# Kernel optimization log

Measured on AMD Instinct MI355X. Metric: run time of the kernel, lower is better.

Reference implementation:

```python
import jax, jax.numpy as jnp
import numpy as np

EPS = 1e-6


def _expand_mask(mask, D, H, W):
    # mask: (B,1,f,f,f) bool -> (B,1,D,H,W) via repeat_interleave on each spatial axis
    m = jnp.repeat(mask, D // mask.shape[2], axis=2)
    m = jnp.repeat(m, H // mask.shape[3], axis=3)
    m = jnp.repeat(m, W // mask.shape[4], axis=4)
    return m


def setup_inputs() -> dict:
    key = jax.random.key(0)
    ks = jax.random.split(key, 10)
    B, C, D, H, W = 2, 192, 32, 32, 32
    K, HID = 7, 4 * C
    x = jax.random.normal(ks[0], (B, C, D, H, W), dtype=jnp.float32)
    mask = jax.random.randint(ks[1], (B, 1, 8, 8, 8), 0, 2) > 0
    dw_w = jax.random.normal(ks[2], (C, 1, K, K, K), dtype=jnp.float32) * (1.0 / np.sqrt(K**3))
    dw_b = jnp.zeros((C,), dtype=jnp.float32)
    ln_w = jnp.ones((C,), dtype=jnp.float32)
    ln_b = jnp.zeros((C,), dtype=jnp.float32)
    w1 = jax.random.normal(ks[3], (C, HID), dtype=jnp.float32) * (1.0 / np.sqrt(C))
    b1 = jnp.zeros((HID,), dtype=jnp.float32)
    w2 = jax.random.normal(ks[4], (HID, C), dtype=jnp.float32) * (1.0 / np.sqrt(HID))
    b2 = jnp.zeros((C,), dtype=jnp.float32)
    gamma = jnp.full((C,), 1e-6, dtype=jnp.float32)
    return {"x": x, "mask": mask, "dw_w": dw_w, "dw_b": dw_b, "ln_w": ln_w,
            "ln_b": ln_b, "w1": w1, "b1": b1, "w2": w2, "b2": b2, "gamma": gamma}


def reference(x, mask, dw_w, dw_b, ln_w, ln_b, w1, b1, w2, b2, gamma):
    B, C, D, H, W = x.shape
    m = _expand_mask(mask, D, H, W)              # (B,1,D,H,W) bool
    mf = m.astype(x.dtype)

    # depthwise 3D conv, SAME padding (padding = kernel//2), groups = C
    y = jax.lax.conv_general_dilated(
        x, dw_w, window_strides=(1, 1, 1), padding='SAME',
        dimension_numbers=('NCDHW', 'OIDHW', 'NCDHW'),
        feature_group_count=C)
    y = y + dw_b[None, :, None, None, None]

    # channels_last: (B,D,H,W,C)
    y = jnp.transpose(y, (0, 2, 3, 4, 1))

    # sparse LayerNorm over channel dim: normalize all tokens, keep only active
    # (equivalent to gather->LN->scatter-into-zeros in the original)
    mu = jnp.mean(y, axis=-1, keepdims=True)
    var = jnp.mean(jnp.square(y - mu), axis=-1, keepdims=True)
    ln = (y - mu) * jax.lax.rsqrt(var + EPS) * ln_w + ln_b
    ln = ln * jnp.transpose(mf, (0, 2, 3, 4, 1))  # zero inactive tokens

    # pointwise MLP
    h = jax.nn.gelu(jnp.einsum('bdhwc,ce->bdhwe', ln, w1) + b1, approximate=False)
    o = jnp.einsum('bdhwe,ec->bdhwc', h, w2) + b2
    o = gamma * o

    # back to channels_first and final sparse mask
    o = jnp.transpose(o, (0, 4, 1, 2, 3)) * mf
    return o
```

## Files before the change

### kernel.cpp

```cpp
#include <hip/hip_runtime.h>
#include <hip/hip_bf16.h>

typedef __attribute__((ext_vector_type(2))) float f2v;
typedef __attribute__((ext_vector_type(4))) float f4v;
typedef __attribute__((ext_vector_type(8))) short bf8v;
typedef __attribute__((ext_vector_type(8))) _Float16 h8v;

#define NPOS 32768
#define CCH  192
#define HID  768

#define WS_Y    ((size_t)0)
#define WS_B1F  ((size_t)25165824)
#define WS_B2F  ((size_t)25460736)
#define WS_WPF  ((size_t)25755648)
#define WS_B3F  ((size_t)26056704)
#define WS_TOTAL_MFMA ((size_t)35690496)
#define WS_TOTAL_DOT2 ((size_t)26056704)

__device__ inline unsigned short f2bf(float f){
  unsigned int u = __float_as_uint(f);
  u += 0x7FFFu + ((u >> 16) & 1u);
  return (unsigned short)(u >> 16);
}
__device__ inline float bf2f(unsigned short s){
  return __uint_as_float(((unsigned int)s) << 16);
}
__device__ inline float gelu_f(float x){
  float u = 0.7978845608028654f * x * fmaf(0.044715f, x*x, 1.0f);
  float e = __expf(2.0f*u);
  float th = __fdividef(e - 1.0f, e + 1.0f);
  return 0.5f*x*(1.0f + th);
}

#define DOT2(A, X, W) \
  asm("v_dot2_f32_f16 %0, %1, %2, %0" : "+v"(A) : "v"(X), "s"(W))

__global__ __launch_bounds__(256) void compact_kernel(
    const int* __restrict__ mask, int* __restrict__ list)
{
  __shared__ unsigned short cnt[256];
  __shared__ int pref[257];
  int t = threadIdx.x;
  int m[4], c0 = 0;
  #pragma unroll
  for (int i = 0; i < 4; ++i) { m[i] = mask[t*4 + i]; c0 += (m[i] != 0); }
  cnt[t] = (unsigned short)c0;
  __syncthreads();
  if (t == 0) {
    int s = 0;
    for (int i = 0; i < 256; ++i) { pref[i] = s; s += cnt[i]; }
    pref[256] = s;
  }
  __syncthreads();
  int na = pref[256];
  int pa = pref[t];
  int pi = na + (t*4 - pref[t]);
  #pragma unroll
  for (int i = 0; i < 4; ++i) {
    if (m[i]) list[pa++] = t*4 + i;
    else      list[pi++] = t*4 + i;
  }
  if (t == 0) list[1024] = na;
}

#define ZSTR 712
__global__ __launch_bounds__(256) void conv_mfma_kernel(
    const float* __restrict__ x, const float* __restrict__ dw_b,
    const unsigned short* __restrict__ b3f, unsigned short* __restrict__ yc)
{
  __shared__ unsigned short tile[22*ZSTR];

  int bid = blockIdx.x;
  int c = bid % 192;
  int r = bid / 192;
  int xq = r & 1, yq = (r >> 1) & 1, zh = (r >> 2) & 1, b = r >> 3;
  int tx0 = xq*16, ty0 = yq*16, zb = zh*16;

  int tid = threadIdx.x;
  const float* xsrc = x + ((size_t)(b*CCH + c))*NPOS;

  #pragma unroll
  for (int it = 0; it < 8; ++it) {
    int idx = tid + 256*it;
    if (idx < 1936) {
      int ci = idx & 3;
      int row = idx >> 2;
      int lz = row / 22, ly = row - lz*22;
      int gz = zb - 3 + lz, gy = ty0 - 3 + ly;
      f4v v0 = {0.f,0.f,0.f,0.f}, v1 = {0.f,0.f,0.f,0.f};
      if (((unsigned)gz < 32u) & ((unsigned)gy < 32u) & (ci < 3)) {
        int gx0 = tx0 - 4 + 8*ci;
        const float* src = xsrc + (size_t)gz*1024 + gy*32;
        if ((unsigned)gx0 <= 28u)     v0 = *(const f4v*)(src + gx0);
        if ((unsigned)(gx0+4) <= 28u) v1 = *(const f4v*)(src + gx0 + 4);
      }
      h8v pk;
      pk[0] = (_Float16)v0[0]; pk[1] = (_Float16)v0[1];
      pk[2] = (_Float16)v0[2]; pk[3] = (_Float16)v0[3];
      pk[4] = (_Float16)v1[0]; pk[5] = (_Float16)v1[1];
      pk[6] = (_Float16)v1[2]; pk[7] = (_Float16)v1[3];
      *(h8v*)(tile + lz*ZSTR + ly*32 + ci*8) = pk;
    }
  }
  __syncthreads();

  int wv = tid >> 6, lane = tid & 63;
  int q = lane >> 4, zm = lane & 15;

  const unsigned short* abase = tile + (size_t)zm*ZSTR + q*8;
  const unsigned short* bbase = b3f + ((size_t)c*49)*512 + (size_t)lane*8;

  f4v acc[4];
  #pragma unroll
  for (int t = 0; t < 4; ++t) acc[t] = (f4v){0.f,0.f,0.f,0.f};

  #pragma unroll 1
  for (int kz = 0; kz < 7; ++kz) {
    h8v Bt[7];
    #pragma unroll
    for (int ky = 0; ky < 7; ++ky)
      Bt[ky] = *(const h8v*)(bbase + (size_t)(kz*7 + ky)*512);
    h8v Af[10];
    #pragma unroll
    for (int rr = 0; rr < 10; ++rr)
      Af[rr] = *(const h8v*)(abase + kz*ZSTR + (4*wv + rr)*32);
    #pragma unroll
    for (int ky = 0; ky < 7; ++ky) {
      acc[0] = __builtin_amdgcn_mfma_f32_16x16x32_f16(Af[ky+0], Bt[ky], acc[0], 0, 0, 0);
      acc[1] = __builtin_amdgcn_mfma_f32_16x16x32_f16(Af[ky+1], Bt[ky], acc[1], 0, 0, 0);
      acc[2] = __builtin_amdgcn_mfma_f32_16x16x32_f16(Af[ky+2], Bt[ky], acc[2], 0, 0, 0);
      acc[3] = __builtin_amdgcn_mfma_f32_16x16x32_f16(Af[ky+3], Bt[ky], acc[3], 0, 0, 0);
    }
  }

  float bias = dw_b[c];
  int cz = zh*4 + q;
  int cx = (tx0 >> 2) + (zm >> 2);
  int xr = zm & 3;
  int cy = (ty0 >> 2) + wv;
  int cell = cz*64 + cy*8 + cx;
  unsigned short* yb0 = yc + (((size_t)(b*512 + cell))*192 + c)*64 + xr;
  #pragma unroll
  for (int t = 0; t < 4; ++t) {
    unsigned short* yb = yb0 + t*4;
    yb[0]  = f2bf(acc[t][0] + bias);
    yb[16] = f2bf(acc[t][1] + bias);
    yb[32] = f2bf(acc[t][2] + bias);
    yb[48] = f2bf(acc[t][3] + bias);
  }
}

__global__ __launch_bounds__(256, 6) void conv_dw_f16_kernel(
    const float* __restrict__ x, const float* __restrict__ dw_b,
    const unsigned int* __restrict__ wpf, unsigned short* __restrict__ yc)
{
  __shared__ unsigned short ring[22*528];

  int bid = blockIdx.x;
  int c = bid % 192;
  int r = bid / 192;
  int xq = r & 1, yq = (r >> 1) & 1, zh = (r >> 2) & 1, b = r >> 3;
  int tx0 = xq*16, ty0 = yq*16, zb = zh*16;

  int tid = threadIdx.x;
  const float* xsrc = x + ((size_t)(b*CCH + c))*NPOS;

  for (int idx = tid; idx < 2904; idx += 256) {
    int sl = idx / 132;
    int rem = idx - sl*132;
    int rr = rem / 6, ci = rem - rr*6;
    int zi = zb - 3 + sl, gy = ty0 - 3 + rr, gx = tx0 - 4 + 4*ci;
    f4v v = {0.f, 0.f, 0.f, 0.f};
    if ((unsigned)zi < 32u && (unsigned)gy < 32u && (unsigned)gx <= 28u)
      v = *(const f4v*)(xsrc + (size_t)zi*1024 + gy*32 + gx);
    union { _Float16 h[4]; uint2 u2; } pk;
    pk.h[0] = (_Float16)v[0]; pk.h[1] = (_Float16)v[1];
    pk.h[2] = (_Float16)v[2]; pk.h[3] = (_Float16)v[3];
    *(uint2*)(ring + sl*528 + rr*24 + ci*4) = pk.u2;
  }
  __syncthreads();

  int p = tid & 15, zl = tid >> 4;
  int px = p & 3, py = p >> 2;
  int y0 = py*4, px4 = px*4;
  const unsigned short* base = ring + zl*528 + y0*24 + px4;
  const unsigned int* wb = wpf + (size_t)c*392;

  float acc[4][4];
  #pragma unroll
  for (int i = 0; i < 4; ++i)
    #pragma unroll
    for (int j = 0; j < 4; ++j) acc[i][j] = 0.f;

  #pragma unroll 1
  for (int s = 0; s < 7; ++s) {
    const unsigned short* sb = base + s*528;
    const unsigned int* wrow = wb + s*56;
    #pragma unroll
    for (int rr = 0; rr < 10; ++rr) {
      const unsigned short* rb = sb + rr*24;
      uint2 q0 = *(const uint2*)(rb);
      uint2 q1 = *(const uint2*)(rb + 4);
      uint2 q2 = *(const uint2*)(rb + 8);
      unsigned int D[6] = {q0.x, q0.y, q1.x, q1.y, q2.x, q2.y};
      #pragma unroll
      for (int dy = 0; dy < 4; ++dy) {
        int ky = rr - dy;
        if (ky < 0 || ky > 6) continue;
        const unsigned int* wk = wrow + ky*8;
        #pragma unroll
        for (int t = 0; t < 4; ++t) {
          DOT2(acc[dy][0], D[t],   wk[t]);
          DOT2(acc[dy][1], D[t+1], wk[4+t]);
          DOT2(acc[dy][2], D[t+1], wk[t]);
          DOT2(acc[dy][3], D[t+2], wk[4+t]);
        }
      }
    }
  }

  float bias = dw_b[c];
  int z = zb + zl;
  int cz = z >> 2, cx = (tx0 >> 2) + px, cy = (ty0 >> 2) + py;
  int cell = cz*64 + cy*8 + cx;
  unsigned short* ybase = yc + (((size_t)(b*512 + cell))*192 + c)*64;
  int tokz = (z & 3)*16;
  #pragma unroll
  for (int dy = 0; dy < 4; ++dy) {
    ushort4 o;
    o.x = f2bf(acc[dy][0] + bias);
    o.y = f2bf(acc[dy][1] + bias);
    o.z = f2bf(acc[dy][2] + bias);
    o.w = f2bf(acc[dy][3] + bias);
    *(ushort4*)(ybase + tokz + dy*4) = o;
  }
}

__global__ __launch_bounds__(256) void conv_dw_f32_kernel(
    const float* __restrict__ x, const float* __restrict__ dw_w,
    const float* __restrict__ dw_b, unsigned short* __restrict__ yc)
{
  __shared__ float ring[22*528];

  int bid = blockIdx.x;
  int c = bid % 192;
  int r = bid / 192;
  int xq = r & 1, yq = (r >> 1) & 1, zh = (r >> 2) & 1, b = r >> 3;
  int tx0 = xq*16, ty0 = yq*16, zb = zh*16;

  int tid = threadIdx.x;
  const float* xsrc = x + ((size_t)(b*CCH + c))*NPOS;

  for (int idx = tid; idx < 2904; idx += 256) {
    int sl = idx / 132;
    int rem = idx - sl*132;
    int rr = rem / 6, ci = rem - rr*6;
    int zi = zb - 3 + sl, gy = ty0 - 3 + rr, gx = tx0 - 4 + 4*ci;
    f4v v = {0.f, 0.f, 0.f, 0.f};
    if ((unsigned)zi < 32u && (unsigned)gy < 32u && (unsigned)gx <= 28u)
      v = *(const f4v*)(xsrc + (size_t)zi*1024 + gy*32 + gx);
    *(f4v*)(ring + sl*528 + rr*24 + ci*4) = v;
  }
  __syncthreads();

  int p = tid & 15, zl = tid >> 4;
  int px = p & 3, py = p >> 2;
  int y0 = py*4, px4 = px*4;
  const float* base = ring + zl*528 + y0*24 + px4;
  const float* wbase = dw_w + (size_t)c*343;

  f2v acc[8];
  #pragma unroll
  for (int i = 0; i < 8; ++i) acc[i] = (f2v){0.f, 0.f};

  #pragma unroll 1
  for (int s = 0; s < 7; ++s) {
    const float* sb = base + s*528;
    f4v n0 = *(const f4v*)(sb);
    f4v n1 = *(const f4v*)(sb + 4);
    f4v n2 = *(const f4v*)(sb + 8);
    #pragma unroll
    for (int rr = 0; rr < 10; ++rr) {
      f4v r0 = n0, r1 = n1, r2 = n2;
      if (rr < 9) {
        n0 = *(const f4v*)(sb + (rr+1)*24);
        n1 = *(const f4v*)(sb + (rr+1)*24 + 4);
        n2 = *(const f4v*)(sb + (rr+1)*24 + 8);
      }
      f2v pr[10];
      pr[1] = (f2v){r0[1], r0[2]};
      pr[2] = (f2v){r0[2], r0[3]};
      pr[3] = (f2v){r0[3], r1[0]};
      pr[4] = (f2v){r1[0], r1[1]};
      pr[5] = (f2v){r1[1], r1[2]};
      pr[6] = (f2v){r1[2], r1[3]};
      pr[7] = (f2v){r1[3], r2[0]};
      pr[8] = (f2v){r2[0], r2[1]};
      pr[9] = (f2v){r2[1], r2[2]};
      #pragma unroll
      for (int dy = 0; dy < 4; ++dy) {
        int ky = rr - dy;
        if (ky < 0 || ky > 6) continue;
        #pragma unroll
        for (int kx = 0; kx < 7; ++kx) {
          float w = wbase[s*49 + ky*7 + kx];
          f2v wv = (f2v){w, w};
          acc[dy*2+0] = __builtin_elementwise_fma(wv, pr[kx+1], acc[dy*2+0]);
          acc[dy*2+1] = __builtin_elementwise_fma(wv, pr[kx+3], acc[dy*2+1]);
        }
      }
    }
  }

  float bias = dw_b[c];
  int z = zb + zl;
  int cz = z >> 2, cx = (tx0 >> 2) + px, cy = (ty0 >> 2) + py;
  int cell = cz*64 + cy*8 + cx;
  unsigned short* ybase = yc + (((size_t)(b*512 + cell))*192 + c)*64;
  int tokz = (z & 3)*16;
  #pragma unroll
  for (int dy = 0; dy < 4; ++dy) {
    ushort4 o;
    o.x = f2bf(acc[dy*2+0][0] + bias);
    o.y = f2bf(acc[dy*2+0][1] + bias);
    o.z = f2bf(acc[dy*2+1][0] + bias);
    o.w = f2bf(acc[dy*2+1][1] + bias);
    *(ushort4*)(ybase + tokz + dy*4) = o;
  }
}

__global__ __launch_bounds__(256) void prep_w_kernel(
    const float* __restrict__ w1, const float* __restrict__ w2,
    const float* __restrict__ dw_w,
    unsigned short* __restrict__ b1f, unsigned short* __restrict__ b2f,
    unsigned int* __restrict__ wpf, unsigned short* __restrict__ b3f)
{
  int gid = blockIdx.x*256 + threadIdx.x;
  if (gid < 18432) {
    int fi = gid;
    int lane = fi & 63, fr = fi >> 6;
    int nt = fr / 6, ks = fr - nt*6;
    int n  = nt*16 + (lane & 15);
    int kb = ks*32 + (lane >> 4)*8;
    #pragma unroll
    for (int j = 0; j < 8; ++j) b1f[fi*8 + j] = f2bf(w1[(kb+j)*HID + n]);
  } else if (gid < 36864) {
    int fi = gid - 18432;
    int lane = fi & 63, fr = fi >> 6;
    int nt = fr / 24, ks = fr - nt*24;
    int n  = nt*16 + (lane & 15);
    int kb = ks*32 + (lane >> 4)*8;
    #pragma unroll
    for (int j = 0; j < 8; ++j) b2f[fi*8 + j] = f2bf(w2[(kb+j)*CCH + n]);
  } else if (gid < 46272) {
    int ci = gid - 36864;
    int cch = ci / 49, t7 = ci - cch*49;
    const float* wr = dw_w + cch*343 + t7*7;
    float w[8];
    #pragma unroll
    for (int j = 0; j < 7; ++j) w[j] = wr[j];
    w[7] = 0.f;
    union { _Float16 h[2]; unsigned int u; } pk;
    #pragma unroll
    for (int t = 0; t < 4; ++t) {
      pk.h[0] = (t == 0) ? (_Float16)0.f : (_Float16)w[2*t-1];
      pk.h[1] = (_Float16)w[2*t];
      wpf[ci*8 + t] = pk.u;
    }
    #pragma unroll
    for (int t = 0; t < 4; ++t) {
      pk.h[0] = (_Float16)w[2*t];
      pk.h[1] = (_Float16)w[2*t+1];
      wpf[ci*8 + 4 + t] = pk.u;
    }
  } else if (gid < 648384) {
    int fi = gid - 46272;
    int lane = fi & 63, frag = fi >> 6;
    int cch = frag / 49, tap = frag - cch*49;
    const float* wr = dw_w + cch*343 + tap*7;
    int q = lane >> 4, n = lane & 15;
    h8v pk;
    #pragma unroll
    for (int j = 0; j < 8; ++j) {
      int t = q*8 + j - n - 1;
      pk[j] = (t >= 0 && t <= 6) ? (_Float16)wr[t] : (_Float16)0.f;
    }
    *(h8v*)(b3f + (size_t)fi*8) = pk;
  }
}

template<int COMPACT>
__global__ __launch_bounds__(256) void mlp_kernel(
    const unsigned short* __restrict__ yc, const unsigned short* __restrict__ b1f,
    const unsigned short* __restrict__ b2f, const float* __restrict__ b1,
    const float* __restrict__ b2, const float* __restrict__ gamma,
    const float* __restrict__ ln_w, const float* __restrict__ ln_b,
    const int* __restrict__ mask, const int* __restrict__ list,
    float* __restrict__ out)
{
  int bid = blockIdx.x;
  int cid, active;
  if constexpr (COMPACT) {
    int na = list[1024];
    cid = list[bid];
    active = bid < na;
  } else {
    cid = bid;
    active = (mask[bid] != 0);
  }
  int b = cid >> 9, cell = cid & 511;
  int cz = cell >> 6, cy = (cell >> 3) & 7, cx = cell & 7;
  int z0 = cz*4, y0 = cy*4, x0 = cx*4;
  int tid = threadIdx.x, wave = tid >> 6, lane = tid & 63;
  int lq = lane >> 4, ln15 = lane & 15;

  if (!active) {
    f4v z4 = {0.f, 0.f, 0.f, 0.f};
    #pragma unroll
    for (int pp = 0; pp < 12; ++pp) {
      int i4 = tid + 256*pp;
      int c = i4 >> 4, rem = i4 & 15;
      int dz = rem >> 2, dy = rem & 3;
      *(f4v*)(out + ((size_t)(b*CCH + c))*NPOS
                  + (size_t)(z0+dz)*1024 + (y0+dy)*32 + x0) = z4;
    }
    return;
  }

  __shared__ __align__(16) char lds[40960];
  unsigned short* hbuf = (unsigned short*)lds;
  float* sred = (float*)lds;
  float* murs = (float*)(lds + 2048);
  unsigned short* aFrag = (unsigned short*)(lds + 16384);

  const unsigned short* ysrc = yc + (size_t)cid*12288;

  {
    int tok = tid & 63, part = tid >> 6;
    float S = 0.f, Q = 0.f;
    #pragma unroll
    for (int j = 0; j < 48; ++j) {
      float v = bf2f(ysrc[(part*48 + j)*64 + tok]);
      S += v; Q = fmaf(v, v, Q);
    }
    sred[part*64 + tok] = S; sred[(4 + part)*64 + tok] = Q;
  }
  __syncthreads();
  if (tid < 64) {
    float S = sred[tid] + sred[64 + tid] + sred[128 + tid] + sred[192 + tid];
    float Q = sred[256 + tid] + sred[320 + tid] + sred[384 + tid] + sred[448 + tid];
    float m = S*(1.f/192.f);
    float var = Q*(1.f/192.f) - m*m;
    murs[tid] = m;
    murs[64 + tid] = rsqrtf(var + 1e-6f);
  }
  __syncthreads();

  #pragma unroll
  for (int k = 0; k < 6; ++k) {
    int fi = tid + 256*k;
    int lane2 = fi & 63, rest = fi >> 6;
    int mt = rest / 6, ks = rest - mt*6;
    int tok = mt*16 + (lane2 & 15);
    int cc0 = ks*32 + (lane2 >> 4)*8;
    float m = murs[tok], rs = murs[64 + tok];
    f4v lw0 = *(const f4v*)(ln_w + cc0), lw1 = *(const f4v*)(ln_w + cc0 + 4);
    f4v lb0 = *(const f4v*)(ln_b + cc0), lb1 = *(const f4v*)(ln_b + cc0 + 4);
    union { bf8v v; unsigned short u[8]; } pk;
    #pragma unroll
    for (int j = 0; j < 4; ++j) {
      float v0 = (bf2f(ysrc[(cc0+j)*64 + tok])   - m)*rs*lw0[j] + lb0[j];
      float v1 = (bf2f(ysrc[(cc0+4+j)*64 + tok]) - m)*rs*lw1[j] + lb1[j];
      pk.u[j] = f2bf(v0); pk.u[4+j] = f2bf(v1);
    }
    *(bf8v*)(aFrag + fi*8) = pk.v;
  }
  __syncthreads();

  f4v acc2[4][3];
  #pragma unroll
  for (int mt = 0; mt < 4; ++mt)
    #pragma unroll
    for (int nt = 0; nt < 3; ++nt)
      acc2[mt][nt] = (f4v){0.f, 0.f, 0.f, 0.f};

  const unsigned short* p1base = b1f + wave*2*3072 + lane*8;
  const unsigned short* p2base = b2f + wave*3*12288 + lane*8;

  bf8v B1r[12];
  #pragma unroll
  for (int i = 0; i < 12; ++i) {
    int jj = i / 6, ks = i - jj*6;
    B1r[i] = *(const bf8v*)(p1base + jj*3072 + ks*512);
  }

  #pragma unroll 1
  for (int ch = 0; ch < 6; ++ch) {
    bf8v B2r[12];
    const unsigned short* p2 = p2base + ch*2048;
    #pragma unroll
    for (int ks2 = 0; ks2 < 4; ++ks2)
      #pragma unroll
      for (int nt = 0; nt < 3; ++nt)
        B2r[ks2*3 + nt] = *(const bf8v*)(p2 + nt*12288 + ks2*512);

    f4v a1[2][4];
    #pragma unroll
    for (int jj = 0; jj < 2; ++jj)
      #pragma unroll
      for (int mt = 0; mt < 4; ++mt) a1[jj][mt] = (f4v){0.f,0.f,0.f,0.f};
    #pragma unroll
    for (int ks = 0; ks < 6; ++ks) {
      bf8v Af[4];
      #pragma unroll
      for (int mt = 0; mt < 4; ++mt)
        Af[mt] = *(const bf8v*)(aFrag + ((mt*6 + ks)*64 + lane)*8);
      #pragma unroll
      for (int jj = 0; jj < 2; ++jj)
        #pragma unroll
        for (int mt = 0; mt < 4; ++mt)
          a1[jj][mt] = __builtin_amdgcn_mfma_f32_16x16x32_bf16(Af[mt], B1r[jj*6+ks], a1[jj][mt], 0, 0, 0);
    }

    if (ch < 5) {
      const unsigned short* p1 = p1base + (ch+1)*24576;
      #pragma unroll
      for (int i = 0; i < 12; ++i) {
        int jj = i / 6, ks = i - jj*6;
        B1r[i] = *(const bf8v*)(p1 + jj*3072 + ks*512);
      }
    }

    #pragma unroll
    for (int jj = 0; jj < 2; ++jj) {
      float b1v = b1[(ch*8 + wave*2 + jj)*16 + ln15];
      int lane_hi = jj*2 + (ln15 >> 3);
      #pragma unroll
      for (int mt = 0; mt < 4; ++mt)
        #pragma unroll
        for (int rr = 0; rr < 4; ++rr) {
          float g = gelu_f(a1[jj][mt][rr] + b1v);
          int elem = ((mt*4 + wave)*64 + lane_hi*16 + (lq*4 + rr))*8 + (lane & 7);
          hbuf[elem] = f2bf(g);
        }
    }
    __syncthreads();
    #pragma unroll
    for (int ks2 = 0; ks2 < 4; ++ks2) {
      bf8v A2[4];
      #pragma unroll
      for (int mt = 0; mt < 4; ++mt)
        A2[mt] = *(const bf8v*)(hbuf + ((mt*4 + ks2)*64 + lane)*8);
      #pragma unroll
      for (int nt = 0; nt < 3; ++nt)
        #pragma unroll
        for (int mt = 0; mt < 4; ++mt)
          acc2[mt][nt] = __builtin_amdgcn_mfma_f32_16x16x32_bf16(A2[mt], B2r[ks2*3+nt], acc2[mt][nt], 0, 0, 0);
    }
    __syncthreads();
  }

  #pragma unroll
  for (int nt = 0; nt < 3; ++nt) {
    int c = (wave*3 + nt)*16 + ln15;
    float gm = gamma[c], bb = b2[c];
    size_t cbase = ((size_t)(b*CCH + c))*NPOS + (size_t)(y0 + lq)*32 + x0;
    #pragma unroll
    for (int mt = 0; mt < 4; ++mt) {
      f4v o;
      o[0] = gm*(acc2[mt][nt][0] + bb);
      o[1] = gm*(acc2[mt][nt][1] + bb);
      o[2] = gm*(acc2[mt][nt][2] + bb);
      o[3] = gm*(acc2[mt][nt][3] + bb);
      *(f4v*)(out + cbase + (size_t)(z0 + mt)*1024) = o;
    }
  }
}

extern "C" void kernel_launch(void* const* d_in, const int* in_sizes, int n_in,
                              void* d_out, int out_size, void* d_ws, size_t ws_size,
                              hipStream_t stream) {
  const float* x     = (const float*)d_in[0];
  const int*   mask  = (const int*)  d_in[1];
  const float* dw_w  = (const float*)d_in[2];
  const float* dw_b  = (const float*)d_in[3];
  const float* ln_w  = (const float*)d_in[4];
  const float* ln_b  = (const float*)d_in[5];
  const float* w1    = (const float*)d_in[6];
  const float* b1    = (const float*)d_in[7];
  const float* w2    = (const float*)d_in[8];
  const float* b2    = (const float*)d_in[9];
  const float* gamma = (const float*)d_in[10];
  float* out = (float*)d_out;
  char* ws = (char*)d_ws;

  unsigned short* yc  = (unsigned short*)(ws + WS_Y);
  unsigned short* b1f = (unsigned short*)(ws + WS_B1F);
  unsigned short* b2f = (unsigned short*)(ws + WS_B2F);
  unsigned int*   wpf = (unsigned int*)(ws + WS_WPF);
  unsigned short* b3f = (unsigned short*)(ws + WS_B3F);
  int*            lst = (int*)(ws + WS_WPF);

  bool mfma_ok = ws_size >= WS_TOTAL_MFMA;
  bool dot2_ok = ws_size >= WS_TOTAL_DOT2;
  int prep_grid = mfma_ok ? 2533 : (dot2_ok ? 181 : 144);
  prep_w_kernel<<<prep_grid, 256, 0, stream>>>(w1, w2, dw_w, b1f, b2f, wpf, b3f);
  if (mfma_ok) {
    compact_kernel<<<1, 256, 0, stream>>>(mask, lst);
    conv_mfma_kernel<<<3072, 256, 0, stream>>>(x, dw_b, b3f, yc);
    mlp_kernel<1><<<1024, 256, 0, stream>>>(yc, b1f, b2f, b1, b2, gamma, ln_w, ln_b, mask, lst, out);
  } else if (dot2_ok) {
    conv_dw_f16_kernel<<<3072, 256, 0, stream>>>(x, dw_b, wpf, yc);
    mlp_kernel<0><<<1024, 256, 0, stream>>>(yc, b1f, b2f, b1, b2, gamma, ln_w, ln_b, mask, nullptr, out);
  } else {
    conv_dw_f32_kernel<<<3072, 256, 0, stream>>>(x, dw_w, dw_b, yc);
    mlp_kernel<0><<<1024, 256, 0, stream>>>(yc, b1f, b2f, b1, b2, gamma, ln_w, ln_b, mask, nullptr, out);
  }
}
```

Baseline: 233.0 us.

## Use eight waves per MLP block with split-K second GEMM and LDS reduction

Doubles the MLP block to 512 threads. Each wave now computes one hidden 16-column tile per chunk instead of two, and the second GEMM is split over K between wave halves. The two halves' partial accumulators are summed through shared memory before the output is written. The aim is more waves in flight per block to hide latency and fewer registers per wave, at the cost of an extra LDS reduction with barriers and half the waves idle during the output stores.

```diff
diff --git a/kernel.cpp b/kernel.cpp
--- a/kernel.cpp
+++ b/kernel.cpp
@@ -391,7 +391,7 @@
 }
 
 template<int COMPACT>
-__global__ __launch_bounds__(256) void mlp_kernel(
+__global__ __launch_bounds__(512) void mlp_kernel(
     const unsigned short* __restrict__ yc, const unsigned short* __restrict__ b1f,
     const unsigned short* __restrict__ b2f, const float* __restrict__ b1,
     const float* __restrict__ b2, const float* __restrict__ gamma,
@@ -418,8 +418,8 @@
   if (!active) {
     f4v z4 = {0.f, 0.f, 0.f, 0.f};
     #pragma unroll
-    for (int pp = 0; pp < 12; ++pp) {
-      int i4 = tid + 256*pp;
+    for (int pp = 0; pp < 6; ++pp) {
+      int i4 = tid + 512*pp;
       int c = i4 >> 4, rem = i4 & 15;
       int dz = rem >> 2, dy = rem & 3;
       *(f4v*)(out + ((size_t)(b*CCH + c))*NPOS
@@ -431,7 +431,8 @@
   __shared__ __align__(16) char lds[40960];
   unsigned short* hbuf = (unsigned short*)lds;
   float* sred = (float*)lds;
-  float* murs = (float*)(lds + 2048);
+  float* murs = (float*)(lds + 4096);
+  float* redu = (float*)lds;
   unsigned short* aFrag = (unsigned short*)(lds + 16384);
 
   const unsigned short* ysrc = yc + (size_t)cid*12288;
@@ -440,16 +441,17 @@
     int tok = tid & 63, part = tid >> 6;
     float S = 0.f, Q = 0.f;
     #pragma unroll
-    for (int j = 0; j < 48; ++j) {
-      float v = bf2f(ysrc[(part*48 + j)*64 + tok]);
+    for (int j = 0; j < 24; ++j) {
+      float v = bf2f(ysrc[(part*24 + j)*64 + tok]);
       S += v; Q = fmaf(v, v, Q);
     }
-    sred[part*64 + tok] = S; sred[(4 + part)*64 + tok] = Q;
+    sred[part*64 + tok] = S; sred[(8 + part)*64 + tok] = Q;
   }
   __syncthreads();
   if (tid < 64) {
-    float S = sred[tid] + sred[64 + tid] + sred[128 + tid] + sred[192 + tid];
-    float Q = sred[256 + tid] + sred[320 + tid] + sred[384 + tid] + sred[448 + tid];
+    float S = 0.f, Q = 0.f;
+    #pragma unroll
+    for (int p = 0; p < 8; ++p) { S += sred[p*64 + tid]; Q += sred[(8+p)*64 + tid]; }
     float m = S*(1.f/192.f);
     float var = Q*(1.f/192.f) - m*m;
     murs[tid] = m;
@@ -458,8 +460,8 @@
   __syncthreads();
 
   #pragma unroll
-  for (int k = 0; k < 6; ++k) {
-    int fi = tid + 256*k;
+  for (int k = 0; k < 3; ++k) {
+    int fi = tid + 512*k;
     int lane2 = fi & 63, rest = fi >> 6;
     int mt = rest / 6, ks = rest - mt*6;
     int tok = mt*16 + (lane2 & 15);
@@ -485,69 +487,63 @@
     for (int nt = 0; nt < 3; ++nt)
       acc2[mt][nt] = (f4v){0.f, 0.f, 0.f, 0.f};
 
-  const unsigned short* p1base = b1f + wave*2*3072 + lane*8;
-  const unsigned short* p2base = b2f + wave*3*12288 + lane*8;
-
-  bf8v B1r[12];
-  #pragma unroll
-  for (int i = 0; i < 12; ++i) {
-    int jj = i / 6, ks = i - jj*6;
-    B1r[i] = *(const bf8v*)(p1base + jj*3072 + ks*512);
-  }
+  int ks2b = (wave >> 2)*2;
+  int w3 = (wave & 3)*3;
+  int khalf = wave >> 1;
+  int lane_hi = (wave & 1)*2 + (ln15 >> 3);
+
+  const unsigned short* p1base = b1f + wave*6*512 + lane*8;
+  const unsigned short* p2base = b2f + (size_t)w3*12288 + lane*8;
+
+  bf8v B1r[6];
+  #pragma unroll
+  for (int ks = 0; ks < 6; ++ks)
+    B1r[ks] = *(const bf8v*)(p1base + ks*512);
 
   #pragma unroll 1
   for (int ch = 0; ch < 6; ++ch) {
-    bf8v B2r[12];
+    bf8v B2r[6];
     const unsigned short* p2 = p2base + ch*2048;
     #pragma unroll
-    for (int ks2 = 0; ks2 < 4; ++ks2)
+    for (int k2 = 0; k2 < 2; ++k2)
       #pragma unroll
       for (int nt = 0; nt < 3; ++nt)
-        B2r[ks2*3 + nt] = *(const bf8v*)(p2 + nt*12288 + ks2*512);
-
-    f4v a1[2][4];
-    #pragma unroll
-    for (int jj = 0; jj < 2; ++jj)
-      #pragma unroll
-      for (int mt = 0; mt < 4; ++mt) a1[jj][mt] = (f4v){0.f,0.f,0.f,0.f};
+        B2r[k2*3 + nt] = *(const bf8v*)(p2 + nt*12288 + (ks2b + k2)*512);
+
+    f4v a1[4];
+    #pragma unroll
+    for (int mt = 0; mt < 4; ++mt) a1[mt] = (f4v){0.f,0.f,0.f,0.f};
     #pragma unroll
     for (int ks = 0; ks < 6; ++ks) {
-      bf8v Af[4];
-      #pragma unroll
-      for (int mt = 0; mt < 4; ++mt)
-        Af[mt] = *(const bf8v*)(aFrag + ((mt*6 + ks)*64 + lane)*8);
-      #pragma unroll
-      for (int jj = 0; jj < 2; ++jj)
-        #pragma unroll
-        for (int mt = 0; mt < 4; ++mt)
-          a1[jj][mt] = __builtin_amdgcn_mfma_f32_16x16x32_bf16(Af[mt], B1r[jj*6+ks], a1[jj][mt], 0, 0, 0);
+      #pragma unroll
+      for (int mt = 0; mt < 4; ++mt) {
+        bf8v Af = *(const bf8v*)(aFrag + ((mt*6 + ks)*64 + lane)*8);
+        a1[mt] = __builtin_amdgcn_mfma_f32_16x16x32_bf16(Af, B1r[ks], a1[mt], 0, 0, 0);
+      }
     }
 
     if (ch < 5) {
       const unsigned short* p1 = p1base + (ch+1)*24576;
       #pragma unroll
-      for (int i = 0; i < 12; ++i) {
-        int jj = i / 6, ks = i - jj*6;
-        B1r[i] = *(const bf8v*)(p1 + jj*3072 + ks*512);
-      }
-    }
-
-    #pragma unroll
-    for (int jj = 0; jj < 2; ++jj) {
-      float b1v = b1[(ch*8 + wave*2 + jj)*16 + ln15];
-      int lane_hi = jj*2 + (ln15 >> 3);
+      for (int ks = 0; ks < 6; ++ks)
+        B1r[ks] = *(const bf8v*)(p1 + ks*512);
+    }
+
+    {
+      float b1v = b1[(ch*8 + wave)*16 + ln15];
       #pragma unroll
       for (int mt = 0; mt < 4; ++mt)
         #pragma unroll
         for (int rr = 0; rr < 4; ++rr) {
-          float g = gelu_f(a1[jj][mt][rr] + b1v);
-          int elem = ((mt*4 + wave)*64 + lane_hi*16 + (lq*4 + rr))*8 + (lane & 7);
+          float g = gelu_f(a1[mt][rr] + b1v);
+          int elem = ((mt*4 + khalf)*64 + lane_hi*16 + (lq*4 + rr))*8 + (lane & 7);
           hbuf[elem] = f2bf(g);
         }
     }
     __syncthreads();
     #pragma unroll
-    for (int ks2 = 0; ks2 < 4; ++ks2) {
+    for (int k2 = 0; k2 < 2; ++k2) {
+      int ks2 = ks2b + k2;
       bf8v A2[4];
       #pragma unroll
       for (int mt = 0; mt < 4; ++mt)
@@ -556,24 +552,50 @@
       for (int nt = 0; nt < 3; ++nt)
         #pragma unroll
         for (int mt = 0; mt < 4; ++mt)
-          acc2[mt][nt] = __builtin_amdgcn_mfma_f32_16x16x32_bf16(A2[mt], B2r[ks2*3+nt], acc2[mt][nt], 0, 0, 0);
+          acc2[mt][nt] = __builtin_amdgcn_mfma_f32_16x16x32_bf16(A2[mt], B2r[k2*3+nt], acc2[mt][nt], 0, 0, 0);
     }
     __syncthreads();
   }
 
   #pragma unroll
-  for (int nt = 0; nt < 3; ++nt) {
-    int c = (wave*3 + nt)*16 + ln15;
-    float gm = gamma[c], bb = b2[c];
-    size_t cbase = ((size_t)(b*CCH + c))*NPOS + (size_t)(y0 + lq)*32 + x0;
-    #pragma unroll
-    for (int mt = 0; mt < 4; ++mt) {
-      f4v o;
-      o[0] = gm*(acc2[mt][nt][0] + bb);
-      o[1] = gm*(acc2[mt][nt][1] + bb);
-      o[2] = gm*(acc2[mt][nt][2] + bb);
-      o[3] = gm*(acc2[mt][nt][3] + bb);
-      *(f4v*)(out + cbase + (size_t)(z0 + mt)*1024) = o;
+  for (int half = 0; half < 2; ++half) {
+    if (wave >= 4) {
+      int base = ((wave - 4)*64 + lane)*24;
+      #pragma unroll
+      for (int m2 = 0; m2 < 2; ++m2)
+        #pragma unroll
+        for (int nt = 0; nt < 3; ++nt)
+          *(f4v*)(redu + base + (m2*3 + nt)*4) = acc2[half*2 + m2][nt];
+    }
+    __syncthreads();
+    if (wave < 4) {
+      int base = (wave*64 + lane)*24;
+      #pragma unroll
+      for (int m2 = 0; m2 < 2; ++m2)
+        #pragma unroll
+        for (int nt = 0; nt < 3; ++nt) {
+          f4v p = *(const f4v*)(redu + base + (m2*3 + nt)*4);
+          acc2[half*2 + m2][nt] += p;
+        }
+    }
+    __syncthreads();
+  }
+
+  if (wave < 4) {
+    #pragma unroll
+    for (int nt = 0; nt < 3; ++nt) {
+      int c = (w3 + nt)*16 + ln15;
+      float gm = gamma[c], bb = b2[c];
+      size_t cbase = ((size_t)(b*CCH + c))*NPOS + (size_t)(y0 + lq)*32 + x0;
+      #pragma unroll
+      for (int mt = 0; mt < 4; ++mt) {
+        f4v o;
+        o[0] = gm*(acc2[mt][nt][0] + bb);
+        o[1] = gm*(acc2[mt][nt][1] + bb);
+        o[2] = gm*(acc2[mt][nt][2] + bb);
+        o[3] = gm*(acc2[mt][nt][3] + bb);
+        *(f4v*)(out + cbase + (size_t)(z0 + mt)*1024) = o;
+      }
     }
   }
 }
@@ -609,12 +631,12 @@
   if (mfma_ok) {
     compact_kernel<<<1, 256, 0, stream>>>(mask, lst);
     conv_mfma_kernel<<<3072, 256, 0, stream>>>(x, dw_b, b3f, yc);
-    mlp_kernel<1><<<1024, 256, 0, stream>>>(yc, b1f, b2f, b1, b2, gamma, ln_w, ln_b, mask, lst, out);
+    mlp_kernel<1><<<1024, 512, 0, stream>>>(yc, b1f, b2f, b1, b2, gamma, ln_w, ln_b, mask, lst, out);
   } else if (dot2_ok) {
     conv_dw_f16_kernel<<<3072, 256, 0, stream>>>(x, dw_b, wpf, yc);
-    mlp_kernel<0><<<1024, 256, 0, stream>>>(yc, b1f, b2f, b1, b2, gamma, ln_w, ln_b, mask, nullptr, out);
+    mlp_kernel<0><<<1024, 512, 0, stream>>>(yc, b1f, b2f, b1, b2, gamma, ln_w, ln_b, mask, nullptr, out);
   } else {
     conv_dw_f32_kernel<<<3072, 256, 0, stream>>>(x, dw_w, dw_b, yc);
-    mlp_kernel<0><<<1024, 256, 0, stream>>>(yc, b1f, b2f, b1, b2, gamma, ln_w, ln_b, mask, nullptr, out);
-  }
-}
+    mlp_kernel<0><<<1024, 512, 0, stream>>>(yc, b1f, b2f, b1, b2, gamma, ln_w, ln_b, mask, nullptr, out);
+  }
+}
```

After: 245.0 us. 1.05x slower.
